# Optimization experiments

Hardware: AMD Instinct MI355X
Metric: run time of the kernel (lower is better)

The kernel has to match this reference:

```python
import jax, jax.numpy as jnp
from jax import lax
import numpy as np

B, T, M, AUX, H, OUT = 256, 256, 8, 32, 64, 1

def setup_inputs() -> dict:
    key = jax.random.key(0)
    ks = jax.random.split(key, 12)
    s_aux = 1.0 / np.sqrt(AUX)
    s_h = 1.0 / np.sqrt(H)
    return {
        "x_m": jax.random.uniform(ks[0], (B, T, M), dtype=jnp.float32),
        "x_a": jax.random.normal(ks[1], (B, T, AUX), dtype=jnp.float32),
        # junction: aux -> (M, H) logits, softmax over H (outgoing mass fractions)
        "Wj": jax.random.uniform(ks[2], (AUX, M * H), jnp.float32, -s_aux, s_aux),
        "bj": jnp.zeros((M * H,), jnp.float32),
        # redistribution: aux -> (H, H) logits, softmax over last dim
        "Wr": jax.random.uniform(ks[3], (AUX, H * H), jnp.float32, -s_aux, s_aux),
        "br": jnp.zeros((H * H,), jnp.float32),
        # out gate: sigmoid(Linear(aux))
        "Wo": jax.random.uniform(ks[4], (AUX, H), jnp.float32, -s_aux, s_aux),
        "bo": jnp.zeros((H,), jnp.float32),
        # final fc: hidden -> out_size
        "Wfc": jax.random.uniform(ks[5], (H, OUT), jnp.float32, -s_h, s_h),
        "bfc": jnp.zeros((OUT,), jnp.float32),
    }


def reference(x_m, x_a, Wj, bj, Wr, br, Wo, bo, Wfc, bfc):
    Bb = x_m.shape[0]

    def step(c, xs):
        xm, xa = xs  # [B, M], [B, AUX]
        j = jax.nn.softmax((xa @ Wj + bj).reshape(Bb, M, H), axis=-1)
        r = jax.nn.softmax((xa @ Wr + br).reshape(Bb, H, H), axis=-1)
        o = jax.nn.sigmoid(xa @ Wo + bo)
        m_in = jnp.einsum('bm,bmh->bh', xm, j)   # inflow distributed to cells
        m_sys = jnp.einsum('bh,bhk->bk', c, r)   # internal redistribution
        m_new = m_in + m_sys
        return m_new, o * m_new                  # (new cell state, output)

    c0 = jnp.zeros((Bb, H), dtype=x_m.dtype)
    xs = (jnp.swapaxes(x_m, 0, 1), jnp.swapaxes(x_a, 0, 1))  # time-major
    c_final, a = lax.scan(step, c0, xs)          # a: [T, B, H]
    out = a[-1] @ Wfc + bfc                      # fc on last timestep output
    return out, c_final
```

## Files before the change

kernel.cpp:

```cpp
#include <hip/hip_runtime.h>


namespace {

constexpr int B_ = 256, T_ = 256, M_ = 8, AUX_ = 32, H_ = 64;
constexpr int NTILE = 288;
constexpr float LOG2E = 1.4426950408889634f;

typedef __fp16 f16x2 __attribute__((ext_vector_type(2)));
typedef __fp16 f16x8 __attribute__((ext_vector_type(8)));
typedef float  f32x4 __attribute__((ext_vector_type(4)));
typedef int    i32x4 __attribute__((ext_vector_type(4)));

union V8 { f16x8 v; f16x2 p[4]; i32x4 i; };

#if __has_builtin(__builtin_amdgcn_exp2f)
#define EXP2(x) __builtin_amdgcn_exp2f(x)
#else
#define EXP2(x) exp2f(x)
#endif

#define MFMA16(A, Bv, C) __builtin_amdgcn_mfma_f32_16x16x32_f16((A), (Bv), (C), 0, 0, 0)

__device__ __forceinline__ float dot2(f16x2 a, f16x2 b, float c) {
    return __builtin_amdgcn_fdot2(a, b, c, false);
}

template <int CTRL>
__device__ __forceinline__ float dpp_add(float v) {
    int t = __builtin_amdgcn_update_dpp(0, __builtin_bit_cast(int, v),
                                        CTRL, 0xf, 0xf, true);
    return v + __builtin_bit_cast(float, t);
}
__device__ __forceinline__ float sum16_all(float v) {
    v = dpp_add<0xB1>(v);
    v = dpp_add<0x4E>(v);
    v = dpp_add<0x141>(v);
    v = dpp_add<0x140>(v);
    return v;
}
__device__ __forceinline__ float sum64_uni(float v) {
    v = dpp_add<0x111>(v); v = dpp_add<0x112>(v); v = dpp_add<0x114>(v);
    v = dpp_add<0x118>(v); v = dpp_add<0x142>(v); v = dpp_add<0x143>(v);
    return __builtin_bit_cast(float,
        __builtin_amdgcn_readlane(__builtin_bit_cast(int, v), 63));
}

__device__ __forceinline__ int pack_pair_rne(float v) {
    const int hv = (int)__builtin_bit_cast(unsigned short, (__fp16)v);
    const int ev = __builtin_amdgcn_update_dpp(0, hv, 0xA0, 0xf, 0xf, true);
    const int ov = __builtin_amdgcn_update_dpp(0, hv, 0xF5, 0xf, 0xf, true);
    return ev | (ov << 16);
}

#define LDS_FENCE() __asm__ volatile("s_waitcnt lgkmcnt(0)" ::: "memory")

__global__ __launch_bounds__(64)
void nomc_prep(const float* __restrict__ Wj, const float* __restrict__ bj,
               const float* __restrict__ Wr, const float* __restrict__ br,
               void* __restrict__ ws)
{
    const int gt = blockIdx.x;
    const int l = threadIdx.x, q = l >> 4, l15 = l & 15;
    const float* src; const float* bsrc; int stride;
    if (gt < 256) { const int n = gt * 16 + l15;        src = Wr + n; bsrc = br + n; stride = 4096; }
    else          { const int n = (gt - 256) * 16 + l15; src = Wj + n; bsrc = bj + n; stride = 512; }
    V8 v;
#pragma unroll
    for (int j = 0; j < 4; ++j) {
        const float f0 = src[(q * 8 + 2 * j)     * stride] * LOG2E;
        const float f1 = src[(q * 8 + 2 * j + 1) * stride] * LOG2E;
        v.p[j] = __builtin_amdgcn_cvt_pkrtz(f0, f1);
    }
    *(i32x4*)((char*)ws + (size_t)gt * 1024 + l * 16) = v.i;
    if (l < 16)
        ((float*)((char*)ws + NTILE * 1024))[gt * 16 + l] = bsrc[0] * LOG2E;
}

#define R_TILE(BF, BV, TT)                                                   \
    do {                                                                     \
        f32x4 acc = {(BV), (BV), (BV), (BV)};                                \
        acc = MFMA16(af.v, (BF).v, acc);                                     \
        const float e0 = EXP2(acc[0]), e1 = EXP2(acc[1]);                    \
        const float e2 = EXP2(acc[2]), e3 = EXP2(acc[3]);                    \
        const int kk = ((TT) << 4) + l15;                                    \
        RT[q * 4 + 0][hb][kk][p] = (__fp16)e0;                               \
        RT[q * 4 + 1][hb][kk][p] = (__fp16)e1;                               \
        RT[q * 4 + 2][hb][kk][p] = (__fp16)e2;                               \
        RT[q * 4 + 3][hb][kk][p] = (__fp16)e3;                               \
        es0 += e0; es1 += e1; es2 += e2; es3 += e3;                          \
    } while (0)

__global__ __launch_bounds__(1024)
__attribute__((amdgpu_waves_per_eu(4, 4)))
void nomc_main(const float* __restrict__ x_m, const float* __restrict__ x_a,
               const float* __restrict__ Wo, const float* __restrict__ bo,
               const float* __restrict__ Wfc, const float* __restrict__ bfc,
               const void* __restrict__ ws, float* __restrict__ out)
{
    const int b = blockIdx.x, tid = threadIdx.x;
    const int w = tid >> 6, l = tid & 63, q = l >> 4, l15 = l & 15;

    __shared__ __align__(16) __fp16 RT[16][8][64][8];
    __shared__ __align__(16) __fp16 JT[16][64][8];
    __shared__ float sinv[16][64];
    __shared__ __align__(16) __fp16 xj[16][8];
    __shared__ __align__(16) __fp16 minL[16][64];
    __shared__ float xm_lds[T_][M_];
    __shared__ float cfin_lds[H_];
    __shared__ float ph[16][16];

    {
        const float* xmb = x_m + (size_t)b * T_ * M_;
        for (int i = tid; i < T_ * M_; i += 1024) (&xm_lds[0][0])[i] = xmb[i];
    }
    __syncthreads();

    const char* wsb = (const char*)ws;
    const float* wbias = (const float*)(wsb + NTILE * 1024);
    const int a_sh = w >> 1;
    const int tb = (w & 1) ? 2 : 0;

    const int sx = q << 1;

    V8 tj0, tj1; float bj0, bj1;
    {
        const int gtj = (64 + a_sh) * 4 + tb;
        tj0.i = *(const i32x4*)(wsb + (size_t)(gtj + 0) * 1024 + l * 16);
        tj1.i = *(const i32x4*)(wsb + (size_t)(gtj + 1) * 1024 + l * 16);
        bj0 = wbias[(gtj + 0) * 16 + l15];
        bj1 = wbias[(gtj + 1) * 16 + l15];
    }

    V8 rc0, rc1, rc2, rc3; float rb0, rb1, rb2, rb3;
    {
        const int gt0 = (w * 4) * 4;
        rc0.i = *(const i32x4*)(wsb + (size_t)(gt0 + 0) * 1024 + l * 16);
        rc1.i = *(const i32x4*)(wsb + (size_t)(gt0 + 1) * 1024 + l * 16);
        rc2.i = *(const i32x4*)(wsb + (size_t)(gt0 + 2) * 1024 + l * 16);
        rc3.i = *(const i32x4*)(wsb + (size_t)(gt0 + 3) * 1024 + l * 16);
        rb0 = wbias[(gt0 + 0) * 16 + l15];
        rb1 = wbias[(gt0 + 1) * 16 + l15];
        rb2 = wbias[(gt0 + 2) * 16 + l15];
        rb3 = wbias[(gt0 + 3) * 16 + l15];
    }

    float c0 = 0.f, c1 = 0.f, c2 = 0.f, c3 = 0.f;

    for (int it = 0; it < 16; ++it) {
        V8 af;
        {
            const float* xa = x_a + ((size_t)b * T_ + it * 16 + l15) * AUX_ + q * 8;
            const f32x4 x0 = *(const f32x4*)xa;
            const f32x4 x1 = *(const f32x4*)(xa + 4);
            af.p[0] = __builtin_amdgcn_cvt_pkrtz(x0.x, x0.y);
            af.p[1] = __builtin_amdgcn_cvt_pkrtz(x0.z, x0.w);
            af.p[2] = __builtin_amdgcn_cvt_pkrtz(x1.x, x1.y);
            af.p[3] = __builtin_amdgcn_cvt_pkrtz(x1.z, x1.w);
        }

        {
            float ej0 = 0.f, ej1 = 0.f, ej2 = 0.f, ej3 = 0.f;
            const int mp = a_sh ^ sx;
#pragma unroll
            for (int s = 0; s < 2; ++s) {
                const int tt = tb + s;
                const float bv = (s == 0) ? bj0 : bj1;
                f32x4 acc = {bv, bv, bv, bv};
                acc = MFMA16(af.v, (s == 0) ? tj0.v : tj1.v, acc);
                const float e0 = EXP2(acc[0]), e1 = EXP2(acc[1]);
                const float e2 = EXP2(acc[2]), e3 = EXP2(acc[3]);
                const int kk = (tt << 4) + l15;
                JT[q * 4 + 0][kk][mp] = (__fp16)e0;
                JT[q * 4 + 1][kk][mp] = (__fp16)e1;
                JT[q * 4 + 2][kk][mp] = (__fp16)e2;
                JT[q * 4 + 3][kk][mp] = (__fp16)e3;
                ej0 += e0; ej1 += e1; ej2 += e2; ej3 += e3;
            }
            ej0 = sum16_all(ej0); ej1 = sum16_all(ej1);
            ej2 = sum16_all(ej2); ej3 = sum16_all(ej3);
            if (l15 == 0) {
                ph[w][q * 4 + 0] = ej0;
                ph[w][q * 4 + 1] = ej1;
                ph[w][q * 4 + 2] = ej2;
                ph[w][q * 4 + 3] = ej3;
            }
        }
        __syncthreads();

        if ((w & 1) == 0 && l15 == 0) {
#pragma unroll
            for (int r = 0; r < 4; ++r) {
                const int t = q * 4 + r;
                const float tot = ph[w][t] + ph[w + 1][t];
                xj[t][a_sh ^ sx] =
                    (__fp16)(xm_lds[it * 16 + t][a_sh] * __builtin_amdgcn_rcpf(tot));
            }
        }

#pragma unroll 1
        for (int g = 0; g < 4; ++g) {
            const int gg = w * 4 + g;
            const int gtn = (w * 4 + ((g + 1) & 3)) * 4;
            V8 n0, n1, n2, n3; float a0, a1, a2, a3;
            n0.i = *(const i32x4*)(wsb + (size_t)(gtn + 0) * 1024 + l * 16);
            n1.i = *(const i32x4*)(wsb + (size_t)(gtn + 1) * 1024 + l * 16);
            n2.i = *(const i32x4*)(wsb + (size_t)(gtn + 2) * 1024 + l * 16);
            n3.i = *(const i32x4*)(wsb + (size_t)(gtn + 3) * 1024 + l * 16);
            a0 = wbias[(gtn + 0) * 16 + l15];
            a1 = wbias[(gtn + 1) * 16 + l15];
            a2 = wbias[(gtn + 2) * 16 + l15];
            a3 = wbias[(gtn + 3) * 16 + l15];
            const int hb = gg >> 3, p = (gg & 7) ^ sx;
            float es0 = 0.f, es1 = 0.f, es2 = 0.f, es3 = 0.f;
            R_TILE(rc0, rb0, 0);
            R_TILE(rc1, rb1, 1);
            R_TILE(rc2, rb2, 2);
            R_TILE(rc3, rb3, 3);
            const float sr0 = sum16_all(es0), sr1 = sum16_all(es1);
            const float sr2 = sum16_all(es2), sr3 = sum16_all(es3);
            if (l15 == 0) {
                sinv[q * 4 + 0][gg] = __builtin_amdgcn_rcpf(sr0);
                sinv[q * 4 + 1][gg] = __builtin_amdgcn_rcpf(sr1);
                sinv[q * 4 + 2][gg] = __builtin_amdgcn_rcpf(sr2);
                sinv[q * 4 + 3][gg] = __builtin_amdgcn_rcpf(sr3);
            }
            rc0 = n0; rc1 = n1; rc2 = n2; rc3 = n3;
            rb0 = a0; rb1 = a1; rb2 = a2; rb3 = a3;
        }
        __syncthreads();

        {
            V8 jv; jv.v = *(const f16x8*)&JT[w][l][0];
            V8 xv; xv.v = *(const f16x8*)&xj[w][0];
            float s = 0.f;
            s = dot2(jv.p[0], xv.p[0], s);
            s = dot2(jv.p[1], xv.p[1], s);
            s = dot2(jv.p[2], xv.p[2], s);
            s = dot2(jv.p[3], xv.p[3], s);
            minL[w][l] = (__fp16)s;
        }
        __syncthreads();

        if (w == 15) {
            const int ab = q << 5;
            for (int u = 0; u < 16; ++u) {
                const int sig = (u >> 2) & 3;
                const float mi0 = (float)minL[u][l15];
                const float mi1 = (float)minL[u][16 + l15];
                const float mi2 = (float)minL[u][32 + l15];
                const float mi3 = (float)minL[u][48 + l15];
                const float svl = sinv[u][l];
                V8 b00, b01, b10, b11, b20, b21, b30, b31;
                b00.v = *(const f16x8*)&RT[u][q][l15][0];
                b01.v = *(const f16x8*)&RT[u][4 + q][l15][0];
                b10.v = *(const f16x8*)&RT[u][q][16 + l15][0];
                b11.v = *(const f16x8*)&RT[u][4 + q][16 + l15][0];
                b20.v = *(const f16x8*)&RT[u][q][32 + l15][0];
                b21.v = *(const f16x8*)&RT[u][4 + q][32 + l15][0];
                b30.v = *(const f16x8*)&RT[u][q][48 + l15][0];
                b31.v = *(const f16x8*)&RT[u][4 + q][48 + l15][0];
                const float cown = (q == 0) ? c0 : (q == 1) ? c1 : (q == 2) ? c2 : c3;
                const int spk = pack_pair_rne(cown * svl);
                V8 A0f, A1f;
                A0f.i[0] = __builtin_amdgcn_ds_bpermute(ab + ((0 ^ sig) << 3), spk);
                A0f.i[1] = __builtin_amdgcn_ds_bpermute(ab + ((1 ^ sig) << 3), spk);
                A0f.i[2] = __builtin_amdgcn_ds_bpermute(ab + ((2 ^ sig) << 3), spk);
                A0f.i[3] = __builtin_amdgcn_ds_bpermute(ab + ((3 ^ sig) << 3), spk);
                A1f.i[0] = __builtin_amdgcn_ds_bpermute(128 + ab + ((0 ^ sig) << 3), spk);
                A1f.i[1] = __builtin_amdgcn_ds_bpermute(128 + ab + ((1 ^ sig) << 3), spk);
                A1f.i[2] = __builtin_amdgcn_ds_bpermute(128 + ab + ((2 ^ sig) << 3), spk);
                A1f.i[3] = __builtin_amdgcn_ds_bpermute(128 + ab + ((3 ^ sig) << 3), spk);
                f32x4 a0 = {mi0, mi0, mi0, mi0};
                a0 = MFMA16(A0f.v, b00.v, a0);
                a0 = MFMA16(A1f.v, b01.v, a0);
                f32x4 a1 = {mi1, mi1, mi1, mi1};
                a1 = MFMA16(A0f.v, b10.v, a1);
                a1 = MFMA16(A1f.v, b11.v, a1);
                f32x4 a2 = {mi2, mi2, mi2, mi2};
                a2 = MFMA16(A0f.v, b20.v, a2);
                a2 = MFMA16(A1f.v, b21.v, a2);
                f32x4 a3 = {mi3, mi3, mi3, mi3};
                a3 = MFMA16(A0f.v, b30.v, a3);
                a3 = MFMA16(A1f.v, b31.v, a3);
                c0 = a0[0]; c1 = a1[0]; c2 = a2[0]; c3 = a3[0];
            }
        }
        __syncthreads();
    }

    if (w == 15) {
        const float cown = (q == 0) ? c0 : (q == 1) ? c1 : (q == 2) ? c2 : c3;
        cfin_lds[l] = cown;
        LDS_FENCE();
        const float* xa = x_a + ((size_t)b * T_ + (T_ - 1)) * AUX_;
        float L = bo[l];
#pragma unroll
        for (int a = 0; a < AUX_; ++a) L = fmaf(xa[a], Wo[a * H_ + l], L);
        const float o = 1.0f / (1.0f + __expf(-L));
        const float cfin = cfin_lds[l];
        float p = (o * cfin) * Wfc[l];
        p = sum64_uni(p);
        if (l == 0) out[b] = p + bfc[0];
        out[B_ + b * H_ + l] = cfin;
    }
}

}

extern "C" void kernel_launch(void* const* d_in, const int* in_sizes, int n_in,
                              void* d_out, int out_size, void* d_ws, size_t ws_size,
                              hipStream_t stream) {
    const float* x_m = (const float*)d_in[0];
    const float* x_a = (const float*)d_in[1];
    const float* Wj  = (const float*)d_in[2];
    const float* bj  = (const float*)d_in[3];
    const float* Wr  = (const float*)d_in[4];
    const float* br  = (const float*)d_in[5];
    const float* Wo  = (const float*)d_in[6];
    const float* bo  = (const float*)d_in[7];
    const float* Wfc = (const float*)d_in[8];
    const float* bfc = (const float*)d_in[9];
    float* out = (float*)d_out;

    hipLaunchKernelGGL(nomc_prep, dim3(NTILE), dim3(64), 0, stream,
                       Wj, bj, Wr, br, d_ws);
    hipLaunchKernelGGL(nomc_main, dim3(B_), dim3(1024), 0, stream,
                       x_m, x_a, Wo, bo, Wfc, bfc, d_ws, out);
}
```

Measured before the change: 234.6 us.

## Software-pipeline junction softmax of next chunk into previous iteration

Moves the junction (J) softmax computation and x_a load for chunk it+1 into the tail of iteration it, so that work runs on waves not busy with the serial recurrence. This removes one __syncthreads per chunk. The J work is also repartitioned: waves 0-13 do pairs of tiles, and wave 14 handles M index 7 alone with four tiles, writing xj directly. Per-iteration J weight tiles are now reloaded from global memory instead of held in registers. This trades register pressure for extra loads and load imbalance.

```diff
diff --git a/kernel.cpp b/kernel.cpp
--- a/kernel.cpp
+++ b/kernel.cpp
@@ -91,8 +91,69 @@
         es0 += e0; es1 += e1; es2 += e2; es3 += e3;                          \
     } while (0)
 
-__global__ __launch_bounds__(1024)
-__attribute__((amdgpu_waves_per_eu(4, 4)))
+#define J_TILE(GT, TT, MP)                                                   \
+    do {                                                                     \
+        V8 bf; bf.i = *(const i32x4*)(wsb + (size_t)(GT) * 1024 + l * 16);   \
+        const float bv = wbias[(GT) * 16 + l15];                             \
+        f32x4 acc = {bv, bv, bv, bv};                                        \
+        acc = MFMA16(af.v, bf.v, acc);                                       \
+        const float e0 = EXP2(acc[0]), e1 = EXP2(acc[1]);                    \
+        const float e2 = EXP2(acc[2]), e3 = EXP2(acc[3]);                    \
+        const int kk = ((TT) << 4) + l15;                                    \
+        JT[q * 4 + 0][kk][(MP)] = (__fp16)e0;                                \
+        JT[q * 4 + 1][kk][(MP)] = (__fp16)e1;                                \
+        JT[q * 4 + 2][kk][(MP)] = (__fp16)e2;                                \
+        JT[q * 4 + 3][kk][(MP)] = (__fp16)e3;                                \
+        ej0 += e0; ej1 += e1; ej2 += e2; ej3 += e3;                          \
+    } while (0)
+
+#define AF_LOAD(ITN)                                                         \
+    do {                                                                     \
+        const float* xa_ = x_a + ((size_t)b * T_ + (ITN) * 16 + l15) * AUX_ + q * 8; \
+        const f32x4 x0_ = *(const f32x4*)xa_;                                \
+        const f32x4 x1_ = *(const f32x4*)(xa_ + 4);                          \
+        af.p[0] = __builtin_amdgcn_cvt_pkrtz(x0_.x, x0_.y);                  \
+        af.p[1] = __builtin_amdgcn_cvt_pkrtz(x0_.z, x0_.w);                  \
+        af.p[2] = __builtin_amdgcn_cvt_pkrtz(x1_.x, x1_.y);                  \
+        af.p[3] = __builtin_amdgcn_cvt_pkrtz(x1_.z, x1_.w);                  \
+    } while (0)
+
+#define J_PAIR()                                                             \
+    do {                                                                     \
+        float ej0 = 0.f, ej1 = 0.f, ej2 = 0.f, ej3 = 0.f;                    \
+        const int mp = a_pr ^ sx;                                            \
+        J_TILE((64 + a_pr) * 4 + tb + 0, tb + 0, mp);                        \
+        J_TILE((64 + a_pr) * 4 + tb + 1, tb + 1, mp);                        \
+        ej0 = sum16_all(ej0); ej1 = sum16_all(ej1);                          \
+        ej2 = sum16_all(ej2); ej3 = sum16_all(ej3);                          \
+        if (l15 == 0) {                                                      \
+            ph[w][q * 4 + 0] = ej0;                                          \
+            ph[w][q * 4 + 1] = ej1;                                          \
+            ph[w][q * 4 + 2] = ej2;                                          \
+            ph[w][q * 4 + 3] = ej3;                                          \
+        }                                                                    \
+    } while (0)
+
+#define J_FULL(ITN)                                                          \
+    do {                                                                     \
+        float ej0 = 0.f, ej1 = 0.f, ej2 = 0.f, ej3 = 0.f;                    \
+        const int mp = 7 ^ sx;                                               \
+        J_TILE(284, 0, mp);                                                  \
+        J_TILE(285, 1, mp);                                                  \
+        J_TILE(286, 2, mp);                                                  \
+        J_TILE(287, 3, mp);                                                  \
+        ej0 = sum16_all(ej0); ej1 = sum16_all(ej1);                          \
+        ej2 = sum16_all(ej2); ej3 = sum16_all(ej3);                          \
+        if (l15 == 0) {                                                      \
+            xj[q * 4 + 0][mp] = (__fp16)(xm_lds[(ITN) * 16 + q * 4 + 0][7] * __builtin_amdgcn_rcpf(ej0)); \
+            xj[q * 4 + 1][mp] = (__fp16)(xm_lds[(ITN) * 16 + q * 4 + 1][7] * __builtin_amdgcn_rcpf(ej1)); \
+            xj[q * 4 + 2][mp] = (__fp16)(xm_lds[(ITN) * 16 + q * 4 + 2][7] * __builtin_amdgcn_rcpf(ej2)); \
+            xj[q * 4 + 3][mp] = (__fp16)(xm_lds[(ITN) * 16 + q * 4 + 3][7] * __builtin_amdgcn_rcpf(ej3)); \
+        }                                                                    \
+    } while (0)
+
+__global__
+__attribute__((amdgpu_flat_work_group_size(1024, 1024), amdgpu_waves_per_eu(4, 4)))
 void nomc_main(const float* __restrict__ x_m, const float* __restrict__ x_a,
                const float* __restrict__ Wo, const float* __restrict__ bo,
                const float* __restrict__ Wfc, const float* __restrict__ bfc,
@@ -118,23 +179,19 @@
 
     const char* wsb = (const char*)ws;
     const float* wbias = (const float*)(wsb + NTILE * 1024);
-    const int a_sh = w >> 1;
+    const int a_pr = w >> 1;
     const int tb = (w & 1) ? 2 : 0;
-
     const int sx = q << 1;
 
-    V8 tj0, tj1; float bj0, bj1;
-    {
-        const int gtj = (64 + a_sh) * 4 + tb;
-        tj0.i = *(const i32x4*)(wsb + (size_t)(gtj + 0) * 1024 + l * 16);
-        tj1.i = *(const i32x4*)(wsb + (size_t)(gtj + 1) * 1024 + l * 16);
-        bj0 = wbias[(gtj + 0) * 16 + l15];
-        bj1 = wbias[(gtj + 1) * 16 + l15];
-    }
+    V8 af;
+    AF_LOAD(0);
+    if (w < 14)       J_PAIR();
+    else if (w == 14) J_FULL(0);
+    __syncthreads();
 
     V8 rc0, rc1, rc2, rc3; float rb0, rb1, rb2, rb3;
     {
-        const int gt0 = (w * 4) * 4;
+        const int gt0 = w * 16;
         rc0.i = *(const i32x4*)(wsb + (size_t)(gt0 + 0) * 1024 + l * 16);
         rc1.i = *(const i32x4*)(wsb + (size_t)(gt0 + 1) * 1024 + l * 16);
         rc2.i = *(const i32x4*)(wsb + (size_t)(gt0 + 2) * 1024 + l * 16);
@@ -148,53 +205,13 @@
     float c0 = 0.f, c1 = 0.f, c2 = 0.f, c3 = 0.f;
 
     for (int it = 0; it < 16; ++it) {
-        V8 af;
-        {
-            const float* xa = x_a + ((size_t)b * T_ + it * 16 + l15) * AUX_ + q * 8;
-            const f32x4 x0 = *(const f32x4*)xa;
-            const f32x4 x1 = *(const f32x4*)(xa + 4);
-            af.p[0] = __builtin_amdgcn_cvt_pkrtz(x0.x, x0.y);
-            af.p[1] = __builtin_amdgcn_cvt_pkrtz(x0.z, x0.w);
-            af.p[2] = __builtin_amdgcn_cvt_pkrtz(x1.x, x1.y);
-            af.p[3] = __builtin_amdgcn_cvt_pkrtz(x1.z, x1.w);
-        }
-
-        {
-            float ej0 = 0.f, ej1 = 0.f, ej2 = 0.f, ej3 = 0.f;
-            const int mp = a_sh ^ sx;
-#pragma unroll
-            for (int s = 0; s < 2; ++s) {
-                const int tt = tb + s;
-                const float bv = (s == 0) ? bj0 : bj1;
-                f32x4 acc = {bv, bv, bv, bv};
-                acc = MFMA16(af.v, (s == 0) ? tj0.v : tj1.v, acc);
-                const float e0 = EXP2(acc[0]), e1 = EXP2(acc[1]);
-                const float e2 = EXP2(acc[2]), e3 = EXP2(acc[3]);
-                const int kk = (tt << 4) + l15;
-                JT[q * 4 + 0][kk][mp] = (__fp16)e0;
-                JT[q * 4 + 1][kk][mp] = (__fp16)e1;
-                JT[q * 4 + 2][kk][mp] = (__fp16)e2;
-                JT[q * 4 + 3][kk][mp] = (__fp16)e3;
-                ej0 += e0; ej1 += e1; ej2 += e2; ej3 += e3;
-            }
-            ej0 = sum16_all(ej0); ej1 = sum16_all(ej1);
-            ej2 = sum16_all(ej2); ej3 = sum16_all(ej3);
-            if (l15 == 0) {
-                ph[w][q * 4 + 0] = ej0;
-                ph[w][q * 4 + 1] = ej1;
-                ph[w][q * 4 + 2] = ej2;
-                ph[w][q * 4 + 3] = ej3;
-            }
-        }
-        __syncthreads();
-
-        if ((w & 1) == 0 && l15 == 0) {
+        if ((w & 1) == 0 && w < 14 && l15 == 0) {
 #pragma unroll
             for (int r = 0; r < 4; ++r) {
                 const int t = q * 4 + r;
                 const float tot = ph[w][t] + ph[w + 1][t];
-                xj[t][a_sh ^ sx] =
-                    (__fp16)(xm_lds[it * 16 + t][a_sh] * __builtin_amdgcn_rcpf(tot));
+                xj[t][a_pr ^ sx] =
+                    (__fp16)(xm_lds[it * 16 + t][a_pr] * __builtin_amdgcn_rcpf(tot));
             }
         }
 
@@ -285,6 +302,11 @@
                 a3 = MFMA16(A1f.v, b31.v, a3);
                 c0 = a0[0]; c1 = a1[0]; c2 = a2[0]; c3 = a3[0];
             }
+            if (it < 15) AF_LOAD(it + 1);
+        } else if (it < 15) {
+            AF_LOAD(it + 1);
+            if (w < 14) J_PAIR();
+            else        J_FULL(it + 1);
         }
         __syncthreads();
     }
```

New measurement: 234.5 us. No clear change (-0.0%).
